# Optimization experiments

Measured on AMD Instinct MI355X. Metric: run time of the kernel, lower is better.

The kernel has to match this reference:

```python
import jax, jax.numpy as jnp
import numpy as np

B, S, H = 2, 1024, 2880
I = 2880
E = 16
K = 4


def setup_inputs() -> dict:
    key = jax.random.key(0)
    ks = jax.random.split(key, 4)
    sc = 0.02  # init scale to keep activations in a sane range
    return {
        "x": jax.random.normal(ks[0], (B, S, H), jnp.float32),
        "gate_w": jax.random.normal(ks[1], (E, H), jnp.float32) * sc,
        "gate_b": jnp.zeros((E,), jnp.float32),
        "w_gate_up": jax.random.normal(ks[2], (E, 2 * I, H), jnp.float32) * sc,
        "b_gate_up": jnp.zeros((E, 2 * I), jnp.float32),
        "w_down": jax.random.normal(ks[3], (E, H, I), jnp.float32) * sc,
        "b_down": jnp.zeros((E, H), jnp.float32),
        "swiglu_alpha": jnp.full((E,), 1.702, jnp.float32),
        "swiglu_beta": jnp.full((E,), 1.0, jnp.float32),
        "swiglu_limit": jnp.full((E,), 7.0, jnp.float32),
    }


def reference(x, gate_w, gate_b, w_gate_up, b_gate_up, w_down, b_down,
              swiglu_alpha, swiglu_beta, swiglu_limit):
    orig_shape = x.shape
    hidden = orig_shape[-1]
    t = x.reshape(-1, hidden)  # [T, H]
    T = t.shape[0]

    # Router: gate linear -> top-k -> renormalize via softmax over selected logits
    logits = t @ gate_w.T + gate_b  # [T, E]
    top_vals, top_idx = jax.lax.top_k(logits, K)  # [T, K]
    top_w = jax.nn.softmax(top_vals, axis=-1)  # RenormalizeMoeRoutingMethod
    # Dense combine matrix [T, E]; zero for non-selected experts
    combine = jnp.zeros((T, E), t.dtype).at[jnp.arange(T)[:, None], top_idx].set(top_w)

    def expert_body(acc, params):
        wgu, bgu, wd, bd, alpha, beta, lim, cw = params
        h = t @ wgu.T + bgu  # [T, 2I] fused gate_up
        glu, lin = jnp.split(h, 2, axis=-1)  # FUSED_GATE_UP_PROJ chunk
        glu = jnp.minimum(glu, lim)  # swiglu_limit clamp (gpt-oss)
        lin = jnp.clip(lin, -lim, lim)
        act = glu * jax.nn.sigmoid(alpha * glu) * (lin + beta)  # [T, I]
        y = act @ wd.T + bd  # [T, H]
        return acc + cw[:, None] * y, None

    init = jnp.zeros((T, hidden), t.dtype)
    out, _ = jax.lax.scan(
        expert_body, init,
        (w_gate_up, b_gate_up, w_down, b_down,
         swiglu_alpha, swiglu_beta, swiglu_limit, combine.T))
    return out.reshape(orig_shape)
```

## Files before the change

### kernel.cpp

```cpp
#include <hip/hip_runtime.h>
#include <stdint.h>
#include <math.h>

#define T_TOK 2048
#define H_DIM 2880
#define I_DIM 2880
#define E_NUM 16
#define TOPK 4

#define BT 256
#define BK 64
#define NK 45
#define MT_MAX 8
#define NT1 45
#define NT2 45

typedef __bf16 bf16_t;
typedef __bf16 bf16x8 __attribute__((ext_vector_type(8)));
typedef __bf16 bf16x4 __attribute__((ext_vector_type(4)));
typedef float f32x4 __attribute__((ext_vector_type(4)));

#define WAITV(N) asm volatile("s_waitcnt vmcnt(" #N ")" ::: "memory")
#define WAITL()  asm volatile("s_waitcnt lgkmcnt(0)" ::: "memory")
#define BAR()    asm volatile("s_barrier" ::: "memory")

__device__ __forceinline__ void gload16(const bf16_t* g, bf16_t* l) {
  __builtin_amdgcn_global_load_lds(
      (__attribute__((address_space(1))) const uint32_t*)g,
      (__attribute__((address_space(3))) uint32_t*)l, 16, 0, 0);
}

__device__ __forceinline__ f32x4 mfma16(bf16x8 a, bf16x8 b, f32x4 c) {
  return __builtin_amdgcn_mfma_f32_16x16x32_bf16(a, b, c, 0, 0, 0);
}

__global__ void k_prep(const float* __restrict__ x, bf16_t* __restrict__ xbf,
                       int* __restrict__ counts) {
  if (blockIdx.x == 0 && threadIdx.x < E_NUM) counts[threadIdx.x] = 0;
  int idx = blockIdx.x * 256 + threadIdx.x;
  const int total = T_TOK * H_DIM / 8;
  if (idx < total) {
    f32x4 a = ((const f32x4*)x)[2 * idx];
    f32x4 b = ((const f32x4*)x)[2 * idx + 1];
    bf16x8 o = {(bf16_t)a[0], (bf16_t)a[1], (bf16_t)a[2], (bf16_t)a[3],
                (bf16_t)b[0], (bf16_t)b[1], (bf16_t)b[2], (bf16_t)b[3]};
    ((bf16x8*)xbf)[idx] = o;
  }
}

__global__ void k_router(const float* __restrict__ x, const float* __restrict__ gw,
                         const float* __restrict__ gb, float* __restrict__ topw,
                         int* __restrict__ counts, int* __restrict__ rowsl) {
  const int t = blockIdx.x;
  const int lane = threadIdx.x;
  const int c = lane >> 4, e = lane & 15;
  const f32x4* x4 = (const f32x4*)(x + (size_t)t * H_DIM);
  const f32x4* w4 = (const f32x4*)(gw + (size_t)e * H_DIM);
  float p = 0.f;
  const int per = (H_DIM / 4) / 4;
  for (int i = c * per; i < (c + 1) * per; ++i) {
    f32x4 xv = x4[i], wv = w4[i];
    p += xv[0] * wv[0] + xv[1] * wv[1] + xv[2] * wv[2] + xv[3] * wv[3];
  }
  p += __shfl_xor(p, 16);
  p += __shfl_xor(p, 32);
  p += gb[e];
  __shared__ float lg[E_NUM];
  if (lane < E_NUM) lg[lane] = p;
  __syncthreads();
  if (lane == 0) {
    float v[E_NUM];
    #pragma unroll
    for (int i = 0; i < E_NUM; ++i) v[i] = lg[i];
    int idxs[TOPK]; float vals[TOPK];
    for (int k = 0; k < TOPK; ++k) {
      int bi = 0; float bv = -1e30f;
      for (int i = 0; i < E_NUM; ++i) {
        if (v[i] > bv) { bv = v[i]; bi = i; }
      }
      idxs[k] = bi; vals[k] = bv; v[bi] = -1e30f;
    }
    float m = vals[0], s = 0.f, w[TOPK];
    for (int k = 0; k < TOPK; ++k) { w[k] = expf(vals[k] - m); s += w[k]; }
    for (int k = 0; k < TOPK; ++k) {
      int slot = t * TOPK + k;
      topw[slot] = w[k] / s;
      int pos = atomicAdd(&counts[idxs[k]], 1);
      rowsl[idxs[k] * T_TOK + pos] = slot;
    }
  }
}


#define G_STAGE_T(KT, BUF) do {                                         \
    int c1_ = (KT) > (NK - 1) ? (NK - 1) : (KT);                        \
    _Pragma("unroll")                                                   \
    for (int i_ = 0; i_ < 4; ++i_)                                      \
      gload16(tsrc[i_] + c1_ * BK, &sT[BUF][wv * 2048 + i_ * 512]);     \
  } while (0)

#define G1_MFMA(CUR) do {                                               \
    _Pragma("unroll")                                                   \
    for (int ks = 0; ks < 2; ++ks) {                                    \
      const int koff = ks * 32 + (lane >> 4) * 8;                       \
      bf16x8 wg_[2], wl_[2], tf[4];                                     \
      _Pragma("unroll")                                                 \
      for (int wi = 0; wi < 2; ++wi) {                                  \
        int rg = 32 * wm + 16 * wi + (lane & 15);                       \
        int swz = koff ^ ((rg & 7) << 3);                               \
        wg_[wi] = *(const bf16x8*)(&sW[CUR][rg * 64 + swz]);            \
        wl_[wi] = *(const bf16x8*)(&sW[CUR][(rg + 64) * 64 + swz]);     \
      }                                                                 \
      _Pragma("unroll")                                                 \
      for (int tj = 0; tj < 4; ++tj) {                                  \
        int rt = 64 * wt + 16 * tj + (lane & 15);                       \
        tf[tj] = *(const bf16x8*)(&sT[CUR][rt * 64 + (koff ^ ((rt & 7) << 3))]); \
      }                                                                 \
      _Pragma("unroll")                                                 \
      for (int wi = 0; wi < 2; ++wi)                                    \
        _Pragma("unroll")                                               \
        for (int tj = 0; tj < 4; ++tj) {                                \
          accg[wi][tj] = mfma16(wg_[wi], tf[tj], accg[wi][tj]);         \
          accl[wi][tj] = mfma16(wl_[wi], tf[tj], accl[wi][tj]);         \
        }                                                               \
    }                                                                   \
  } while (0)

#define G1_ITER(KK, WSET) do {                                          \
    const int cur_ = (KK) & 1;                                          \
    G_STAGE_T((KK) + 1, cur_ ^ 1);                                      \
    _Pragma("unroll")                                                   \
    for (int p_ = 0; p_ < 4; ++p_) {                                    \
      bf16x4 b_ = {(bf16_t)WSET[p_][0], (bf16_t)WSET[p_][1],            \
                   (bf16_t)WSET[p_][2], (bf16_t)WSET[p_][3]};           \
      *(bf16x4*)(&sW[cur_ ^ 1][wo[p_]]) = b_;                           \
    }                                                                   \
    { int c3_ = (KK) + 3 > (NK - 1) ? (NK - 1) : (KK) + 3;              \
      _Pragma("unroll")                                                 \
      for (int p_ = 0; p_ < 4; ++p_)                                    \
        WSET[p_] = *(const f32x4*)(wbase + wgo[p_] + c3_ * BK); }       \
    __builtin_amdgcn_s_setprio(1);                                      \
    G1_MFMA(cur_);                                                      \
    __builtin_amdgcn_s_setprio(0);                                      \
    WAITV(4); WAITL(); BAR();                                           \
  } while (0)

__global__ __launch_bounds__(512, 2)
void k_gemm1(const bf16_t* __restrict__ xbf, const float* __restrict__ wgu,
             const float* __restrict__ bgu, const float* __restrict__ al,
             const float* __restrict__ be, const float* __restrict__ lim_,
             const int* __restrict__ counts, const int* __restrict__ rowsl,
             bf16_t* __restrict__ act) {
  const int nwg = E_NUM * NT1 * MT_MAX;
  const int L = (blockIdx.x & 7) * (nwg >> 3) + (blockIdx.x >> 3);
  const int mt = L & (MT_MAX - 1);
  const int t2 = L >> 3;
  const int nt = t2 % NT1;
  const int e  = t2 / NT1;
  const int Ne = counts[e];
  const int m0 = mt * BT;
  if (m0 >= Ne) return;
  const int n0 = nt * 64;

  __shared__ alignas(16) bf16_t sW[2][128 * 64];
  __shared__ alignas(16) bf16_t sT[2][256 * 64];

  const int tid = threadIdx.x;
  const int wv = tid >> 6, lane = tid & 63;
  const int wm = wv & 1, wt = wv >> 1;
  const int* rl = rowsl + e * T_TOK;

  const bf16_t* tsrc[4];
  {
    const int r_ = lane >> 3, cc = lane & 7;
    #pragma unroll
    for (int i = 0; i < 4; ++i) {
      int r = wv * 32 + i * 8 + r_;
      int li = m0 + r; if (li > Ne - 1) li = Ne - 1;
      int tok = rl[li] >> 2;
      tsrc[i] = xbf + (size_t)tok * H_DIM + ((cc ^ (r_ & 7)) << 3);
    }
  }

  const int wrow = tid >> 4, wf = tid & 15;
  const float* wbase = wgu + (size_t)e * (2 * I_DIM) * H_DIM + wf * 4;
  int wgo[4], wo[4];
  #pragma unroll
  for (int p = 0; p < 4; ++p) {
    int row = wrow + p * 32;
    int grow = (row < 64) ? (n0 + row) : (I_DIM + n0 + row - 64);
    wgo[p] = grow * H_DIM;
    wo[p] = row * 64 + ((wf * 4) ^ ((row & 7) << 3));
  }

  f32x4 zero = {0.f, 0.f, 0.f, 0.f};
  f32x4 accg[2][4], accl[2][4];
  #pragma unroll
  for (int i = 0; i < 2; ++i)
    #pragma unroll
    for (int j = 0; j < 4; ++j) { accg[i][j] = zero; accl[i][j] = zero; }

  f32x4 wA[4], wB[4];
  #pragma unroll
  for (int p = 0; p < 4; ++p) wA[p] = *(const f32x4*)(wbase + wgo[p]);
  WAITV(0);
  #pragma unroll
  for (int p = 0; p < 4; ++p) {
    bf16x4 b = {(bf16_t)wA[p][0], (bf16_t)wA[p][1],
                (bf16_t)wA[p][2], (bf16_t)wA[p][3]};
    *(bf16x4*)(&sW[0][wo[p]]) = b;
  }
  G_STAGE_T(0, 0);
  #pragma unroll
  for (int p = 0; p < 4; ++p) wA[p] = *(const f32x4*)(wbase + wgo[p] + 1 * BK);
  #pragma unroll
  for (int p = 0; p < 4; ++p) wB[p] = *(const f32x4*)(wbase + wgo[p] + 2 * BK);
  WAITV(4);
  WAITL(); BAR();

  for (int kb = 0; kb < NK - 1; kb += 2) {
    G1_ITER(kb, wA);
    G1_ITER(kb + 1, wB);
  }
  G1_ITER(NK - 1, wA);

  const float alpha = al[e], beta = be[e], lim = lim_[e];
  const float* bgp = bgu + (size_t)e * (2 * I_DIM);
  #pragma unroll
  for (int wi = 0; wi < 2; ++wi) {
    const int nb = n0 + 32 * wm + 16 * wi + ((lane >> 4) << 2);
    f32x4 bg4 = *(const f32x4*)(bgp + nb);
    f32x4 bl4 = *(const f32x4*)(bgp + I_DIM + nb);
    #pragma unroll
    for (int tj = 0; tj < 4; ++tj) {
      const int li2 = m0 + 64 * wt + 16 * tj + (lane & 15);
      if (li2 < Ne) {
        const int slot = rl[li2];
        bf16x4 ov;
        #pragma unroll
        for (int r = 0; r < 4; ++r) {
          float g = accg[wi][tj][r] + bg4[r];
          float l = accl[wi][tj][r] + bl4[r];
          g = fminf(g, lim);
          l = fminf(fmaxf(l, -lim), lim);
          float sg = 1.0f / (1.0f + expf(-alpha * g));
          ov[r] = (bf16_t)(g * sg * (l + beta));
        }
        *(bf16x4*)(&act[(size_t)slot * I_DIM + nb]) = ov;
      }
    }
  }
}


#define G2_MFMA(CUR) do {                                               \
    _Pragma("unroll")                                                   \
    for (int ks = 0; ks < 2; ++ks) {                                    \
      const int koff = ks * 32 + (lane >> 4) * 8;                       \
      bf16x8 wf_[2], tf[4];                                             \
      _Pragma("unroll")                                                 \
      for (int wi = 0; wi < 2; ++wi) {                                  \
        int rg = 32 * wm + 16 * wi + (lane & 15);                       \
        wf_[wi] = *(const bf16x8*)(&sW[CUR][rg * 64 + (koff ^ ((rg & 7) << 3))]); \
      }                                                                 \
      _Pragma("unroll")                                                 \
      for (int tj = 0; tj < 4; ++tj) {                                  \
        int rt = 64 * wt + 16 * tj + (lane & 15);                       \
        tf[tj] = *(const bf16x8*)(&sT[CUR][rt * 64 + (koff ^ ((rt & 7) << 3))]); \
      }                                                                 \
      _Pragma("unroll")                                                 \
      for (int wi = 0; wi < 2; ++wi)                                    \
        _Pragma("unroll")                                               \
        for (int tj = 0; tj < 4; ++tj)                                  \
          acc[wi][tj] = mfma16(wf_[wi], tf[tj], acc[wi][tj]);           \
    }                                                                   \
  } while (0)

#define G2_ITER(KK, WSET) do {                                          \
    const int cur_ = (KK) & 1;                                          \
    G_STAGE_T((KK) + 1, cur_ ^ 1);                                      \
    _Pragma("unroll")                                                   \
    for (int p_ = 0; p_ < 2; ++p_) {                                    \
      bf16x4 b_ = {(bf16_t)WSET[p_][0], (bf16_t)WSET[p_][1],            \
                   (bf16_t)WSET[p_][2], (bf16_t)WSET[p_][3]};           \
      *(bf16x4*)(&sW[cur_ ^ 1][wo[p_]]) = b_;                           \
    }                                                                   \
    { int c3_ = (KK) + 3 > (NK - 1) ? (NK - 1) : (KK) + 3;              \
      _Pragma("unroll")                                                 \
      for (int p_ = 0; p_ < 2; ++p_)                                    \
        WSET[p_] = *(const f32x4*)(wbase + wgo[p_] + c3_ * BK); }       \
    __builtin_amdgcn_s_setprio(1);                                      \
    G2_MFMA(cur_);                                                      \
    __builtin_amdgcn_s_setprio(0);                                      \
    WAITV(2); WAITL(); BAR();                                           \
  } while (0)

__global__ __launch_bounds__(512, 4)
void k_gemm2(const bf16_t* __restrict__ act, const float* __restrict__ wd,
             const float* __restrict__ bd, const float* __restrict__ topw,
             const int* __restrict__ counts, const int* __restrict__ rowsl,
             float* __restrict__ ybuf) {
  const int nwg = E_NUM * NT2 * MT_MAX;
  const int L = (blockIdx.x & 7) * (nwg >> 3) + (blockIdx.x >> 3);
  const int mt = L & (MT_MAX - 1);
  const int t2 = L >> 3;
  const int ht = t2 % NT2;
  const int e  = t2 / NT2;
  const int Ne = counts[e];
  const int m0 = mt * BT;
  if (m0 >= Ne) return;
  const int h0 = ht * 64;

  __shared__ alignas(16) bf16_t sW[2][64 * 64];
  __shared__ alignas(16) bf16_t sT[2][256 * 64];

  const int tid = threadIdx.x;
  const int wv = tid >> 6, lane = tid & 63;
  const int wm = wv & 1, wt = wv >> 1;
  const int* rl = rowsl + e * T_TOK;

  const bf16_t* tsrc[4];
  {
    const int r_ = lane >> 3, cc = lane & 7;
    #pragma unroll
    for (int i = 0; i < 4; ++i) {
      int r = wv * 32 + i * 8 + r_;
      int li = m0 + r; if (li > Ne - 1) li = Ne - 1;
      int slot = rl[li];
      tsrc[i] = act + (size_t)slot * I_DIM + ((cc ^ (r_ & 7)) << 3);
    }
  }

  const int wrow = tid >> 4, wf = tid & 15;
  const float* wbase = wd + (size_t)e * H_DIM * I_DIM + wf * 4;
  int wgo[2], wo[2];
  #pragma unroll
  for (int p = 0; p < 2; ++p) {
    int row = wrow + p * 32;
    wgo[p] = (h0 + row) * I_DIM;
    wo[p] = row * 64 + ((wf * 4) ^ ((row & 7) << 3));
  }

  f32x4 zero = {0.f, 0.f, 0.f, 0.f};
  f32x4 acc[2][4];
  #pragma unroll
  for (int i = 0; i < 2; ++i)
    #pragma unroll
    for (int j = 0; j < 4; ++j) acc[i][j] = zero;

  f32x4 wA[2], wB[2];
  #pragma unroll
  for (int p = 0; p < 2; ++p) wA[p] = *(const f32x4*)(wbase + wgo[p]);
  WAITV(0);
  #pragma unroll
  for (int p = 0; p < 2; ++p) {
    bf16x4 b = {(bf16_t)wA[p][0], (bf16_t)wA[p][1],
                (bf16_t)wA[p][2], (bf16_t)wA[p][3]};
    *(bf16x4*)(&sW[0][wo[p]]) = b;
  }
  G_STAGE_T(0, 0);
  #pragma unroll
  for (int p = 0; p < 2; ++p) wA[p] = *(const f32x4*)(wbase + wgo[p] + 1 * BK);
  #pragma unroll
  for (int p = 0; p < 2; ++p) wB[p] = *(const f32x4*)(wbase + wgo[p] + 2 * BK);
  WAITV(2);
  WAITL(); BAR();

  for (int kb = 0; kb < NK - 1; kb += 2) {
    G2_ITER(kb, wA);
    G2_ITER(kb + 1, wB);
  }
  G2_ITER(NK - 1, wA);

  const float* bdp = bd + (size_t)e * H_DIM;
  #pragma unroll
  for (int wi = 0; wi < 2; ++wi) {
    const int hb = h0 + 32 * wm + 16 * wi + ((lane >> 4) << 2);
    f32x4 b4 = *(const f32x4*)(bdp + hb);
    #pragma unroll
    for (int tj = 0; tj < 4; ++tj) {
      const int li2 = m0 + 64 * wt + 16 * tj + (lane & 15);
      if (li2 < Ne) {
        const int slot = rl[li2];
        const float tw = topw[slot];
        f32x4 o = (acc[wi][tj] + b4) * tw;
        *(f32x4*)(&ybuf[(size_t)slot * H_DIM + hb]) = o;
      }
    }
  }
}

__global__ void k_combine(const float* __restrict__ ybuf, float* __restrict__ out) {
  const int j4 = H_DIM / 4;
  int idx = blockIdx.x * 256 + threadIdx.x;
  if (idx >= T_TOK * j4) return;
  int t = idx / j4, j = idx - t * j4;
  const f32x4* yb = (const f32x4*)ybuf;
  f32x4 s = yb[(size_t)(t * 4 + 0) * j4 + j];
  s = s + yb[(size_t)(t * 4 + 1) * j4 + j];
  s = s + yb[(size_t)(t * 4 + 2) * j4 + j];
  s = s + yb[(size_t)(t * 4 + 3) * j4 + j];
  ((f32x4*)out)[idx] = s;
}

extern "C" void kernel_launch(void* const* d_in, const int* in_sizes, int n_in,
                              void* d_out, int out_size, void* d_ws, size_t ws_size,
                              hipStream_t stream) {
  const float* x   = (const float*)d_in[0];
  const float* gw  = (const float*)d_in[1];
  const float* gb  = (const float*)d_in[2];
  const float* wgu = (const float*)d_in[3];
  const float* bgu = (const float*)d_in[4];
  const float* wd  = (const float*)d_in[5];
  const float* bd  = (const float*)d_in[6];
  const float* sal = (const float*)d_in[7];
  const float* sbe = (const float*)d_in[8];
  const float* sli = (const float*)d_in[9];
  float* out = (float*)d_out;

  char* ws = (char*)d_ws;
  int*    counts = (int*)(ws + 0);
  int*    rowsl  = (int*)(ws + 4096);
  float*  topw   = (float*)(ws + 4096 + 131072);
  bf16_t* xbf    = (bf16_t*)(ws + (1 << 20));
  bf16_t* act    = (bf16_t*)(ws + (size_t)(16 << 20));
  float*  ybuf   = (float*)(ws + (size_t)(64 << 20));

  k_prep<<<dim3(2880), dim3(256), 0, stream>>>(x, xbf, counts);
  k_router<<<dim3(T_TOK), dim3(64), 0, stream>>>(x, gw, gb, topw, counts, rowsl);
  k_gemm1<<<dim3(E_NUM * NT1 * MT_MAX), dim3(512), 0, stream>>>(
      xbf, wgu, bgu, sal, sbe, sli, counts, rowsl, act);
  k_gemm2<<<dim3(E_NUM * NT2 * MT_MAX), dim3(512), 0, stream>>>(
      act, wd, bd, topw, counts, rowsl, ybuf);
  k_combine<<<dim3(5760), dim3(256), 0, stream>>>(ybuf, out);
}
```

Measured before the change: 1.546 ms.

## Shrink GEMM tiles to 128 tokens, K=32, triple-buffer token tiles, new LDS swizzle

Both grouped expert GEMMs move from 256-token, 512-thread tiles with K-step 64 to 128-token, 256-thread tiles with K-step 32. Token tiles are now triple-buffered with a prefetch distance of two steps, under a new LDS swizzle function. The main loop is unrolled by six to rotate the buffers. The aim is less wasted work on partially filled expert tiles, more resident workgroups per CU, and deeper latency hiding. In exchange there are twice as many barriers per K, and the fp32 weights are re-read by more token tiles.

New measurement: 3.890 ms. +151.6%, slower.

```diff
diff --git a/kernel.cpp b/kernel.cpp
--- a/kernel.cpp
+++ b/kernel.cpp
@@ -8,10 +8,10 @@
 #define E_NUM 16
 #define TOPK 4
 
-#define BT 256
-#define BK 64
-#define NK 45
-#define MT_MAX 8
+#define BT 128
+#define BK 32
+#define NK 90
+#define MT_MAX 16
 #define NT1 45
 #define NT2 45
 
@@ -32,6 +32,11 @@
 
 __device__ __forceinline__ f32x4 mfma16(bf16x8 a, bf16x8 b, f32x4 c) {
   return __builtin_amdgcn_mfma_f32_16x16x32_bf16(a, b, c, 0, 0, 0);
+}
+
+__device__ __forceinline__ int ldsoff(int row, int g) {
+  int r = row & 31;
+  return ((row >> 5) << 10) + (((r << 2) + ((g + (r >> 1)) & 3)) << 3);
 }
 
 __global__ void k_prep(const float* __restrict__ x, bf16_t* __restrict__ xbf,
@@ -91,61 +96,56 @@
   }
 }
 
-
 #define G_STAGE_T(KT, BUF) do {                                         \
     int c1_ = (KT) > (NK - 1) ? (NK - 1) : (KT);                        \
     _Pragma("unroll")                                                   \
-    for (int i_ = 0; i_ < 4; ++i_)                                      \
-      gload16(tsrc[i_] + c1_ * BK, &sT[BUF][wv * 2048 + i_ * 512]);     \
+    for (int i_ = 0; i_ < 2; ++i_)                                      \
+      gload16(tsrc[i_] + c1_ * BK, &sT[BUF][wv * 1024 + i_ * 512]);     \
   } while (0)
 
-#define G1_MFMA(CUR) do {                                               \
-    _Pragma("unroll")                                                   \
-    for (int ks = 0; ks < 2; ++ks) {                                    \
-      const int koff = ks * 32 + (lane >> 4) * 8;                       \
-      bf16x8 wg_[2], wl_[2], tf[4];                                     \
-      _Pragma("unroll")                                                 \
-      for (int wi = 0; wi < 2; ++wi) {                                  \
-        int rg = 32 * wm + 16 * wi + (lane & 15);                       \
-        int swz = koff ^ ((rg & 7) << 3);                               \
-        wg_[wi] = *(const bf16x8*)(&sW[CUR][rg * 64 + swz]);            \
-        wl_[wi] = *(const bf16x8*)(&sW[CUR][(rg + 64) * 64 + swz]);     \
-      }                                                                 \
+
+#define G1_MFMA(SWC, STR) do {                                          \
+    const int g_ = lane >> 4, rs_ = lane & 15;                          \
+    bf16x8 wg_[2], wl_[2], tf[4];                                       \
+    _Pragma("unroll")                                                   \
+    for (int wi = 0; wi < 2; ++wi) {                                    \
+      int rg = 32 * wm + 16 * wi + rs_;                                 \
+      wg_[wi] = *(const bf16x8*)(&sW[SWC][ldsoff(rg, g_)]);             \
+      wl_[wi] = *(const bf16x8*)(&sW[SWC][ldsoff(rg + 64, g_)]);        \
+    }                                                                   \
+    _Pragma("unroll")                                                   \
+    for (int tj = 0; tj < 4; ++tj) {                                    \
+      int rt = 64 * wt + 16 * tj + rs_;                                 \
+      tf[tj] = *(const bf16x8*)(&sT[STR][ldsoff(rt, g_)]);              \
+    }                                                                   \
+    _Pragma("unroll")                                                   \
+    for (int wi = 0; wi < 2; ++wi)                                      \
       _Pragma("unroll")                                                 \
       for (int tj = 0; tj < 4; ++tj) {                                  \
-        int rt = 64 * wt + 16 * tj + (lane & 15);                       \
-        tf[tj] = *(const bf16x8*)(&sT[CUR][rt * 64 + (koff ^ ((rt & 7) << 3))]); \
+        accg[wi][tj] = mfma16(wg_[wi], tf[tj], accg[wi][tj]);           \
+        accl[wi][tj] = mfma16(wl_[wi], tf[tj], accl[wi][tj]);           \
       }                                                                 \
-      _Pragma("unroll")                                                 \
-      for (int wi = 0; wi < 2; ++wi)                                    \
-        _Pragma("unroll")                                               \
-        for (int tj = 0; tj < 4; ++tj) {                                \
-          accg[wi][tj] = mfma16(wg_[wi], tf[tj], accg[wi][tj]);         \
-          accl[wi][tj] = mfma16(wl_[wi], tf[tj], accl[wi][tj]);         \
-        }                                                               \
-    }                                                                   \
   } while (0)
 
-#define G1_ITER(KK, WSET) do {                                          \
-    const int cur_ = (KK) & 1;                                          \
-    G_STAGE_T((KK) + 1, cur_ ^ 1);                                      \
+#define G1_ITER(KK, WSET, SWC, STR, STW) do {                           \
+    G_STAGE_T((KK) + 2, STW);                                           \
     _Pragma("unroll")                                                   \
     for (int p_ = 0; p_ < 4; ++p_) {                                    \
       bf16x4 b_ = {(bf16_t)WSET[p_][0], (bf16_t)WSET[p_][1],            \
                    (bf16_t)WSET[p_][2], (bf16_t)WSET[p_][3]};           \
-      *(bf16x4*)(&sW[cur_ ^ 1][wo[p_]]) = b_;                           \
+      *(bf16x4*)(&sW[(SWC) ^ 1][wo[p_]]) = b_;                          \
     }                                                                   \
     { int c3_ = (KK) + 3 > (NK - 1) ? (NK - 1) : (KK) + 3;              \
       _Pragma("unroll")                                                 \
       for (int p_ = 0; p_ < 4; ++p_)                                    \
         WSET[p_] = *(const f32x4*)(wbase + wgo[p_] + c3_ * BK); }       \
     __builtin_amdgcn_s_setprio(1);                                      \
-    G1_MFMA(cur_);                                                      \
+    G1_MFMA(SWC, STR);                                                  \
     __builtin_amdgcn_s_setprio(0);                                      \
-    WAITV(4); WAITL(); BAR();                                           \
+    WAITV(6); WAITL(); BAR();                                           \
   } while (0)
 
-__global__ __launch_bounds__(512, 2)
+__global__ __launch_bounds__(256, 4)
 void k_gemm1(const bf16_t* __restrict__ xbf, const float* __restrict__ wgu,
              const float* __restrict__ bgu, const float* __restrict__ al,
              const float* __restrict__ be, const float* __restrict__ lim_,
@@ -154,7 +154,7 @@
   const int nwg = E_NUM * NT1 * MT_MAX;
   const int L = (blockIdx.x & 7) * (nwg >> 3) + (blockIdx.x >> 3);
   const int mt = L & (MT_MAX - 1);
-  const int t2 = L >> 3;
+  const int t2 = L >> 4;
   const int nt = t2 % NT1;
   const int e  = t2 / NT1;
   const int Ne = counts[e];
@@ -162,35 +162,36 @@
   if (m0 >= Ne) return;
   const int n0 = nt * 64;
 
-  __shared__ alignas(16) bf16_t sW[2][128 * 64];
-  __shared__ alignas(16) bf16_t sT[2][256 * 64];
+  __shared__ alignas(16) bf16_t sW[2][128 * 32];
+  __shared__ alignas(16) bf16_t sT[3][128 * 32];
 
   const int tid = threadIdx.x;
   const int wv = tid >> 6, lane = tid & 63;
   const int wm = wv & 1, wt = wv >> 1;
   const int* rl = rowsl + e * T_TOK;
 
-  const bf16_t* tsrc[4];
+  const bf16_t* tsrc[2];
   {
-    const int r_ = lane >> 3, cc = lane & 7;
-    #pragma unroll
-    for (int i = 0; i < 4; ++i) {
-      int r = wv * 32 + i * 8 + r_;
-      int li = m0 + r; if (li > Ne - 1) li = Ne - 1;
+    #pragma unroll
+    for (int i = 0; i < 2; ++i) {
+      int q = i * 64 + lane;
+      int r = q >> 2;
+      int g = ((q & 3) - (r >> 1)) & 3;
+      int li = m0 + wv * 32 + r; if (li > Ne - 1) li = Ne - 1;
       int tok = rl[li] >> 2;
-      tsrc[i] = xbf + (size_t)tok * H_DIM + ((cc ^ (r_ & 7)) << 3);
-    }
-  }
-
-  const int wrow = tid >> 4, wf = tid & 15;
-  const float* wbase = wgu + (size_t)e * (2 * I_DIM) * H_DIM + wf * 4;
+      tsrc[i] = xbf + (size_t)tok * H_DIM + g * 8;
+    }
+  }
+
+  const int wrow = tid >> 3, wf2 = tid & 7;
+  const float* wbase = wgu + (size_t)e * (2 * I_DIM) * H_DIM + wf2 * 4;
   int wgo[4], wo[4];
   #pragma unroll
   for (int p = 0; p < 4; ++p) {
     int row = wrow + p * 32;
     int grow = (row < 64) ? (n0 + row) : (I_DIM + n0 + row - 64);
     wgo[p] = grow * H_DIM;
-    wo[p] = row * 64 + ((wf * 4) ^ ((row & 7) << 3));
+    wo[p] = ldsoff(row, wf2 >> 1) + (wf2 & 1) * 4;
   }
 
   f32x4 zero = {0.f, 0.f, 0.f, 0.f};
@@ -212,17 +213,21 @@
   }
   G_STAGE_T(0, 0);
   #pragma unroll
-  for (int p = 0; p < 4; ++p) wA[p] = *(const f32x4*)(wbase + wgo[p] + 1 * BK);
+  for (int p = 0; p < 4; ++p) wA[p] = *(const f32x4*)(wbase + wgo[p] + BK);
+  WAITV(0);
+  G_STAGE_T(1, 1);
   #pragma unroll
   for (int p = 0; p < 4; ++p) wB[p] = *(const f32x4*)(wbase + wgo[p] + 2 * BK);
-  WAITV(4);
   WAITL(); BAR();
 
-  for (int kb = 0; kb < NK - 1; kb += 2) {
-    G1_ITER(kb, wA);
-    G1_ITER(kb + 1, wB);
-  }
-  G1_ITER(NK - 1, wA);
+  for (int kb = 0; kb < NK; kb += 6) {
+    G1_ITER(kb + 0, wA, 0, 0, 2);
+    G1_ITER(kb + 1, wB, 1, 1, 0);
+    G1_ITER(kb + 2, wA, 0, 2, 1);
+    G1_ITER(kb + 3, wB, 1, 0, 2);
+    G1_ITER(kb + 4, wA, 0, 1, 0);
+    G1_ITER(kb + 5, wB, 1, 2, 1);
+  }
 
   const float alpha = al[e], beta = be[e], lim = lim_[e];
   const float* bgp = bgu + (size_t)e * (2 * I_DIM);
@@ -253,49 +258,45 @@
 }
 
 
-#define G2_MFMA(CUR) do {                                               \
-    _Pragma("unroll")                                                   \
-    for (int ks = 0; ks < 2; ++ks) {                                    \
-      const int koff = ks * 32 + (lane >> 4) * 8;                       \
-      bf16x8 wf_[2], tf[4];                                             \
+#define G2_MFMA(SWC, STR) do {                                          \
+    const int g_ = lane >> 4, rs_ = lane & 15;                          \
+    bf16x8 wf_[2], tf[4];                                               \
+    _Pragma("unroll")                                                   \
+    for (int wi = 0; wi < 2; ++wi) {                                    \
+      int rg = 32 * wm + 16 * wi + rs_;                                 \
+      wf_[wi] = *(const bf16x8*)(&sW[SWC][ldsoff(rg, g_)]);             \
+    }                                                                   \
+    _Pragma("unroll")                                                   \
+    for (int tj = 0; tj < 4; ++tj) {                                    \
+      int rt = 64 * wt + 16 * tj + rs_;                                 \
+      tf[tj] = *(const bf16x8*)(&sT[STR][ldsoff(rt, g_)]);              \
+    }                                                                   \
+    _Pragma("unroll")                                                   \
+    for (int wi = 0; wi < 2; ++wi)                                      \
       _Pragma("unroll")                                                 \
-      for (int wi = 0; wi < 2; ++wi) {                                  \
-        int rg = 32 * wm + 16 * wi + (lane & 15);                       \
-        wf_[wi] = *(const bf16x8*)(&sW[CUR][rg * 64 + (koff ^ ((rg & 7) << 3))]); \
-      }                                                                 \
-      _Pragma("unroll")                                                 \
-      for (int tj = 0; tj < 4; ++tj) {                                  \
-        int rt = 64 * wt + 16 * tj + (lane & 15);                       \
-        tf[tj] = *(const bf16x8*)(&sT[CUR][rt * 64 + (koff ^ ((rt & 7) << 3))]); \
-      }                                                                 \
-      _Pragma("unroll")                                                 \
-      for (int wi = 0; wi < 2; ++wi)                                    \
-        _Pragma("unroll")                                               \
-        for (int tj = 0; tj < 4; ++tj)                                  \
-          acc[wi][tj] = mfma16(wf_[wi], tf[tj], acc[wi][tj]);           \
-    }                                                                   \
+      for (int tj = 0; tj < 4; ++tj)                                    \
+        acc[wi][tj] = mfma16(wf_[wi], tf[tj], acc[wi][tj]);             \
   } while (0)
 
-#define G2_ITER(KK, WSET) do {                                          \
-    const int cur_ = (KK) & 1;                                          \
-    G_STAGE_T((KK) + 1, cur_ ^ 1);                                      \
+#define G2_ITER(KK, WSET, SWC, STR, STW) do {                           \
+    G_STAGE_T((KK) + 2, STW);                                           \
     _Pragma("unroll")                                                   \
     for (int p_ = 0; p_ < 2; ++p_) {                                    \
       bf16x4 b_ = {(bf16_t)WSET[p_][0], (bf16_t)WSET[p_][1],            \
                    (bf16_t)WSET[p_][2], (bf16_t)WSET[p_][3]};           \
-      *(bf16x4*)(&sW[cur_ ^ 1][wo[p_]]) = b_;                           \
+      *(bf16x4*)(&sW[(SWC) ^ 1][wo[p_]]) = b_;                          \
     }                                                                   \
     { int c3_ = (KK) + 3 > (NK - 1) ? (NK - 1) : (KK) + 3;              \
       _Pragma("unroll")                                                 \
       for (int p_ = 0; p_ < 2; ++p_)                                    \
         WSET[p_] = *(const f32x4*)(wbase + wgo[p_] + c3_ * BK); }       \
     __builtin_amdgcn_s_setprio(1);                                      \
-    G2_MFMA(cur_);                                                      \
+    G2_MFMA(SWC, STR);                                                  \
     __builtin_amdgcn_s_setprio(0);                                      \
-    WAITV(2); WAITL(); BAR();                                           \
+    WAITV(4); WAITL(); BAR();                                           \
   } while (0)
 
-__global__ __launch_bounds__(512, 4)
+__global__ __launch_bounds__(256, 4)
 void k_gemm2(const bf16_t* __restrict__ act, const float* __restrict__ wd,
              const float* __restrict__ bd, const float* __restrict__ topw,
              const int* __restrict__ counts, const int* __restrict__ rowsl,
@@ -303,7 +304,7 @@
   const int nwg = E_NUM * NT2 * MT_MAX;
   const int L = (blockIdx.x & 7) * (nwg >> 3) + (blockIdx.x >> 3);
   const int mt = L & (MT_MAX - 1);
-  const int t2 = L >> 3;
+  const int t2 = L >> 4;
   const int ht = t2 % NT2;
   const int e  = t2 / NT2;
   const int Ne = counts[e];
@@ -311,34 +312,35 @@
   if (m0 >= Ne) return;
   const int h0 = ht * 64;
 
-  __shared__ alignas(16) bf16_t sW[2][64 * 64];
-  __shared__ alignas(16) bf16_t sT[2][256 * 64];
+  __shared__ alignas(16) bf16_t sW[2][64 * 32];
+  __shared__ alignas(16) bf16_t sT[3][128 * 32];
 
   const int tid = threadIdx.x;
   const int wv = tid >> 6, lane = tid & 63;
   const int wm = wv & 1, wt = wv >> 1;
   const int* rl = rowsl + e * T_TOK;
 
-  const bf16_t* tsrc[4];
+  const bf16_t* tsrc[2];
   {
-    const int r_ = lane >> 3, cc = lane & 7;
-    #pragma unroll
-    for (int i = 0; i < 4; ++i) {
-      int r = wv * 32 + i * 8 + r_;
-      int li = m0 + r; if (li > Ne - 1) li = Ne - 1;
+    #pragma unroll
+    for (int i = 0; i < 2; ++i) {
+      int q = i * 64 + lane;
+      int r = q >> 2;
+      int g = ((q & 3) - (r >> 1)) & 3;
+      int li = m0 + wv * 32 + r; if (li > Ne - 1) li = Ne - 1;
       int slot = rl[li];
-      tsrc[i] = act + (size_t)slot * I_DIM + ((cc ^ (r_ & 7)) << 3);
-    }
-  }
-
-  const int wrow = tid >> 4, wf = tid & 15;
-  const float* wbase = wd + (size_t)e * H_DIM * I_DIM + wf * 4;
+      tsrc[i] = act + (size_t)slot * I_DIM + g * 8;
+    }
+  }
+
+  const int wrow = tid >> 3, wf2 = tid & 7;
+  const float* wbase = wd + (size_t)e * H_DIM * I_DIM + wf2 * 4;
   int wgo[2], wo[2];
   #pragma unroll
   for (int p = 0; p < 2; ++p) {
     int row = wrow + p * 32;
     wgo[p] = (h0 + row) * I_DIM;
-    wo[p] = row * 64 + ((wf * 4) ^ ((row & 7) << 3));
+    wo[p] = ldsoff(row, wf2 >> 1) + (wf2 & 1) * 4;
   }
 
   f32x4 zero = {0.f, 0.f, 0.f, 0.f};
@@ -360,17 +362,21 @@
   }
   G_STAGE_T(0, 0);
   #pragma unroll
-  for (int p = 0; p < 2; ++p) wA[p] = *(const f32x4*)(wbase + wgo[p] + 1 * BK);
+  for (int p = 0; p < 2; ++p) wA[p] = *(const f32x4*)(wbase + wgo[p] + BK);
+  WAITV(0);
+  G_STAGE_T(1, 1);
   #pragma unroll
   for (int p = 0; p < 2; ++p) wB[p] = *(const f32x4*)(wbase + wgo[p] + 2 * BK);
-  WAITV(2);
   WAITL(); BAR();
 
-  for (int kb = 0; kb < NK - 1; kb += 2) {
-    G2_ITER(kb, wA);
-    G2_ITER(kb + 1, wB);
-  }
-  G2_ITER(NK - 1, wA);
+  for (int kb = 0; kb < NK; kb += 6) {
+    G2_ITER(kb + 0, wA, 0, 0, 2);
+    G2_ITER(kb + 1, wB, 1, 1, 0);
+    G2_ITER(kb + 2, wA, 0, 2, 1);
+    G2_ITER(kb + 3, wB, 1, 0, 2);
+    G2_ITER(kb + 4, wA, 0, 1, 0);
+    G2_ITER(kb + 5, wB, 1, 2, 1);
+  }
 
   const float* bdp = bd + (size_t)e * H_DIM;
   #pragma unroll
@@ -428,9 +434,9 @@
 
   k_prep<<<dim3(2880), dim3(256), 0, stream>>>(x, xbf, counts);
   k_router<<<dim3(T_TOK), dim3(64), 0, stream>>>(x, gw, gb, topw, counts, rowsl);
-  k_gemm1<<<dim3(E_NUM * NT1 * MT_MAX), dim3(512), 0, stream>>>(
+  k_gemm1<<<dim3(E_NUM * NT1 * MT_MAX), dim3(256), 0, stream>>>(
       xbf, wgu, bgu, sal, sbe, sli, counts, rowsl, act);
-  k_gemm2<<<dim3(E_NUM * NT2 * MT_MAX), dim3(512), 0, stream>>>(
+  k_gemm2<<<dim3(E_NUM * NT2 * MT_MAX), dim3(256), 0, stream>>>(
       act, wd, bd, topw, counts, rowsl, ybuf);
   k_combine<<<dim3(5760), dim3(256), 0, stream>>>(ybuf, out);
 }
```

## Enlarge GEMM N-tiles and use 1024-thread blocks with new LDS swizzle

Applied to the files above, without the earlier changes.

Both expert GEMMs now run with 16 waves per block. The gate_up kernel's weight tile grows from 64 to 96 columns per half (192 rows), and the down kernel's from 64 to 192 output columns. With larger N-tiles, each block re-reads the gathered token rows fewer times, and the fp32 weights are loaded and converted fewer times per token. The LDS layout switches from an XOR swizzle to a rotation-based one (loff) with per-lane global_load_lds addressing. The cost is more LDS per block, higher register pressure from the larger accumulators, and launch bounds of 1024x4 that may not be satisfiable and could force spills or lower occupancy.

Result: faster. 1.465 ms (-5.2%).

```diff
diff --git a/kernel.cpp b/kernel.cpp
--- a/kernel.cpp
+++ b/kernel.cpp
@@ -12,8 +12,8 @@
 #define BK 64
 #define NK 45
 #define MT_MAX 8
-#define NT1 45
-#define NT2 45
+#define NT1 30
+#define NT2 15
 
 typedef __bf16 bf16_t;
 typedef __bf16 bf16x8 __attribute__((ext_vector_type(8)));
@@ -24,7 +24,7 @@
 #define WAITL()  asm volatile("s_waitcnt lgkmcnt(0)" ::: "memory")
 #define BAR()    asm volatile("s_barrier" ::: "memory")
 
-__device__ __forceinline__ void gload16(const bf16_t* g, bf16_t* l) {
+__device__ __forceinline__ void gload16(const void* g, void* l) {
   __builtin_amdgcn_global_load_lds(
       (__attribute__((address_space(1))) const uint32_t*)g,
       (__attribute__((address_space(3))) uint32_t*)l, 16, 0, 0);
@@ -32,6 +32,15 @@
 
 __device__ __forceinline__ f32x4 mfma16(bf16x8 a, bf16x8 b, f32x4 c) {
   return __builtin_amdgcn_mfma_f32_16x16x32_bf16(a, b, c, 0, 0, 0);
+}
+
+__device__ __forceinline__ int loff(int row, int g) {
+  return ((row >> 5) << 11) + ((row & 31) << 6) + (((g + (row & 7)) & 7) << 3);
+}
+
+__device__ __forceinline__ bf16x4 cvt4(f32x4 a) {
+  bf16x4 o = {(bf16_t)a[0], (bf16_t)a[1], (bf16_t)a[2], (bf16_t)a[3]};
+  return o;
 }
 
 __global__ void k_prep(const float* __restrict__ x, bf16_t* __restrict__ xbf,
@@ -91,37 +100,37 @@
   }
 }
 
-
 #define G_STAGE_T(KT, BUF) do {                                         \
     int c1_ = (KT) > (NK - 1) ? (NK - 1) : (KT);                        \
     _Pragma("unroll")                                                   \
-    for (int i_ = 0; i_ < 4; ++i_)                                      \
-      gload16(tsrc[i_] + c1_ * BK, &sT[BUF][wv * 2048 + i_ * 512]);     \
+    for (int i_ = 0; i_ < 2; ++i_)                                      \
+      gload16(tsrc[i_] + c1_ * BK,                                      \
+              &sT[BUF][wv * 1024 + i_ * 512 + lane * 8]);               \
   } while (0)
+
 
 #define G1_MFMA(CUR) do {                                               \
     _Pragma("unroll")                                                   \
     for (int ks = 0; ks < 2; ++ks) {                                    \
-      const int koff = ks * 32 + (lane >> 4) * 8;                       \
-      bf16x8 wg_[2], wl_[2], tf[4];                                     \
-      _Pragma("unroll")                                                 \
-      for (int wi = 0; wi < 2; ++wi) {                                  \
-        int rg = 32 * wm + 16 * wi + (lane & 15);                       \
-        int swz = koff ^ ((rg & 7) << 3);                               \
-        wg_[wi] = *(const bf16x8*)(&sW[CUR][rg * 64 + swz]);            \
-        wl_[wi] = *(const bf16x8*)(&sW[CUR][(rg + 64) * 64 + swz]);     \
+      const int gk = 4 * ks + u;                                        \
+      bf16x8 wg_[3], wl_[3], tf[2];                                     \
+      _Pragma("unroll")                                                 \
+      for (int f = 0; f < 3; ++f) {                                     \
+        int rg = 48 * wo + 16 * f + rs;                                 \
+        wg_[f] = *(const bf16x8*)(&sW[CUR][loff(rg, gk)]);              \
+        wl_[f] = *(const bf16x8*)(&sW[CUR][loff(rg + 96, gk)]);         \
       }                                                                 \
       _Pragma("unroll")                                                 \
-      for (int tj = 0; tj < 4; ++tj) {                                  \
-        int rt = 64 * wt + 16 * tj + (lane & 15);                       \
-        tf[tj] = *(const bf16x8*)(&sT[CUR][rt * 64 + (koff ^ ((rt & 7) << 3))]); \
+      for (int tj = 0; tj < 2; ++tj) {                                  \
+        int rt = 32 * wt + 16 * tj + rs;                                \
+        tf[tj] = *(const bf16x8*)(&sT[CUR][loff(rt, gk)]);              \
       }                                                                 \
       _Pragma("unroll")                                                 \
-      for (int wi = 0; wi < 2; ++wi)                                    \
+      for (int f = 0; f < 3; ++f)                                       \
         _Pragma("unroll")                                               \
-        for (int tj = 0; tj < 4; ++tj) {                                \
-          accg[wi][tj] = mfma16(wg_[wi], tf[tj], accg[wi][tj]);         \
-          accl[wi][tj] = mfma16(wl_[wi], tf[tj], accl[wi][tj]);         \
+        for (int tj = 0; tj < 2; ++tj) {                                \
+          accg[f][tj] = mfma16(wg_[f], tf[tj], accg[f][tj]);            \
+          accl[f][tj] = mfma16(wl_[f], tf[tj], accl[f][tj]);            \
         }                                                               \
     }                                                                   \
   } while (0)
@@ -130,22 +139,19 @@
     const int cur_ = (KK) & 1;                                          \
     G_STAGE_T((KK) + 1, cur_ ^ 1);                                      \
     _Pragma("unroll")                                                   \
-    for (int p_ = 0; p_ < 4; ++p_) {                                    \
-      bf16x4 b_ = {(bf16_t)WSET[p_][0], (bf16_t)WSET[p_][1],            \
-                   (bf16_t)WSET[p_][2], (bf16_t)WSET[p_][3]};           \
-      *(bf16x4*)(&sW[cur_ ^ 1][wo[p_]]) = b_;                           \
-    }                                                                   \
+    for (int p_ = 0; p_ < 3; ++p_)                                      \
+      *(bf16x4*)(&sW[cur_ ^ 1][woff[p_]]) = cvt4(WSET[p_]);             \
     { int c3_ = (KK) + 3 > (NK - 1) ? (NK - 1) : (KK) + 3;              \
       _Pragma("unroll")                                                 \
-      for (int p_ = 0; p_ < 4; ++p_)                                    \
-        WSET[p_] = *(const f32x4*)(wbase + wgo[p_] + c3_ * BK); }       \
+      for (int p_ = 0; p_ < 3; ++p_)                                    \
+        WSET[p_] = *(const f32x4*)(wsrc[p_] + c3_ * BK); }              \
     __builtin_amdgcn_s_setprio(1);                                      \
     G1_MFMA(cur_);                                                      \
     __builtin_amdgcn_s_setprio(0);                                      \
-    WAITV(4); WAITL(); BAR();                                           \
+    WAITV(3); WAITL(); BAR();                                           \
   } while (0)
 
-__global__ __launch_bounds__(512, 2)
+__global__ __launch_bounds__(1024, 4)
 void k_gemm1(const bf16_t* __restrict__ xbf, const float* __restrict__ wgu,
              const float* __restrict__ bgu, const float* __restrict__ al,
              const float* __restrict__ be, const float* __restrict__ lim_,
@@ -160,62 +166,61 @@
   const int Ne = counts[e];
   const int m0 = mt * BT;
   if (m0 >= Ne) return;
-  const int n0 = nt * 64;
-
-  __shared__ alignas(16) bf16_t sW[2][128 * 64];
+  const int n0 = nt * 96;
+
+  __shared__ alignas(16) bf16_t sW[2][192 * 64];
   __shared__ alignas(16) bf16_t sT[2][256 * 64];
 
   const int tid = threadIdx.x;
   const int wv = tid >> 6, lane = tid & 63;
-  const int wm = wv & 1, wt = wv >> 1;
+  const int wt = wv & 7, wo = wv >> 3;
+  const int u = lane >> 4, rs = lane & 15;
   const int* rl = rowsl + e * T_TOK;
 
-  const bf16_t* tsrc[4];
+  const bf16_t* tsrc[2];
   {
-    const int r_ = lane >> 3, cc = lane & 7;
-    #pragma unroll
-    for (int i = 0; i < 4; ++i) {
-      int r = wv * 32 + i * 8 + r_;
-      int li = m0 + r; if (li > Ne - 1) li = Ne - 1;
+    #pragma unroll
+    for (int i = 0; i < 2; ++i) {
+      int q = i * 64 + lane;
+      int row = 16 * wv + (q >> 3);
+      int gd = q & 7;
+      int g = (gd - (row & 7)) & 7;
+      int li = m0 + row; if (li > Ne - 1) li = Ne - 1;
       int tok = rl[li] >> 2;
-      tsrc[i] = xbf + (size_t)tok * H_DIM + ((cc ^ (r_ & 7)) << 3);
+      tsrc[i] = xbf + (size_t)tok * H_DIM + g * 8;
     }
   }
 
   const int wrow = tid >> 4, wf = tid & 15;
-  const float* wbase = wgu + (size_t)e * (2 * I_DIM) * H_DIM + wf * 4;
-  int wgo[4], wo[4];
-  #pragma unroll
-  for (int p = 0; p < 4; ++p) {
-    int row = wrow + p * 32;
-    int grow = (row < 64) ? (n0 + row) : (I_DIM + n0 + row - 64);
-    wgo[p] = grow * H_DIM;
-    wo[p] = row * 64 + ((wf * 4) ^ ((row & 7) << 3));
+  const float* wsrc[3];
+  int woff[3];
+  #pragma unroll
+  for (int p = 0; p < 3; ++p) {
+    int row = 64 * p + wrow;
+    int grow = (row < 96) ? (n0 + row) : (I_DIM + n0 + row - 96);
+    wsrc[p] = wgu + ((size_t)e * 2 * I_DIM + grow) * H_DIM + wf * 4;
+    woff[p] = loff(row, wf >> 1) + (wf & 1) * 4;
   }
 
   f32x4 zero = {0.f, 0.f, 0.f, 0.f};
-  f32x4 accg[2][4], accl[2][4];
-  #pragma unroll
-  for (int i = 0; i < 2; ++i)
-    #pragma unroll
-    for (int j = 0; j < 4; ++j) { accg[i][j] = zero; accl[i][j] = zero; }
-
-  f32x4 wA[4], wB[4];
-  #pragma unroll
-  for (int p = 0; p < 4; ++p) wA[p] = *(const f32x4*)(wbase + wgo[p]);
+  f32x4 accg[3][2], accl[3][2];
+  #pragma unroll
+  for (int i = 0; i < 3; ++i)
+    #pragma unroll
+    for (int j = 0; j < 2; ++j) { accg[i][j] = zero; accl[i][j] = zero; }
+
+  f32x4 wA[3], wB[3];
+  #pragma unroll
+  for (int p = 0; p < 3; ++p) wA[p] = *(const f32x4*)(wsrc[p]);
   WAITV(0);
   #pragma unroll
-  for (int p = 0; p < 4; ++p) {
-    bf16x4 b = {(bf16_t)wA[p][0], (bf16_t)wA[p][1],
-                (bf16_t)wA[p][2], (bf16_t)wA[p][3]};
-    *(bf16x4*)(&sW[0][wo[p]]) = b;
-  }
+  for (int p = 0; p < 3; ++p) *(bf16x4*)(&sW[0][woff[p]]) = cvt4(wA[p]);
   G_STAGE_T(0, 0);
   #pragma unroll
-  for (int p = 0; p < 4; ++p) wA[p] = *(const f32x4*)(wbase + wgo[p] + 1 * BK);
-  #pragma unroll
-  for (int p = 0; p < 4; ++p) wB[p] = *(const f32x4*)(wbase + wgo[p] + 2 * BK);
-  WAITV(4);
+  for (int p = 0; p < 3; ++p) wA[p] = *(const f32x4*)(wsrc[p] + BK);
+  #pragma unroll
+  for (int p = 0; p < 3; ++p) wB[p] = *(const f32x4*)(wsrc[p] + 2 * BK);
+  WAITV(3);
   WAITL(); BAR();
 
   for (int kb = 0; kb < NK - 1; kb += 2) {
@@ -227,20 +232,20 @@
   const float alpha = al[e], beta = be[e], lim = lim_[e];
   const float* bgp = bgu + (size_t)e * (2 * I_DIM);
   #pragma unroll
-  for (int wi = 0; wi < 2; ++wi) {
-    const int nb = n0 + 32 * wm + 16 * wi + ((lane >> 4) << 2);
+  for (int f = 0; f < 3; ++f) {
+    const int nb = n0 + 48 * wo + 16 * f + 4 * u;
     f32x4 bg4 = *(const f32x4*)(bgp + nb);
     f32x4 bl4 = *(const f32x4*)(bgp + I_DIM + nb);
     #pragma unroll
-    for (int tj = 0; tj < 4; ++tj) {
-      const int li2 = m0 + 64 * wt + 16 * tj + (lane & 15);
+    for (int tj = 0; tj < 2; ++tj) {
+      const int li2 = m0 + 32 * wt + 16 * tj + rs;
       if (li2 < Ne) {
         const int slot = rl[li2];
         bf16x4 ov;
         #pragma unroll
         for (int r = 0; r < 4; ++r) {
-          float g = accg[wi][tj][r] + bg4[r];
-          float l = accl[wi][tj][r] + bl4[r];
+          float g = accg[f][tj][r] + bg4[r];
+          float l = accl[f][tj][r] + bl4[r];
           g = fminf(g, lim);
           l = fminf(fmaxf(l, -lim), lim);
           float sg = 1.0f / (1.0f + expf(-alpha * g));
@@ -256,23 +261,23 @@
 #define G2_MFMA(CUR) do {                                               \
     _Pragma("unroll")                                                   \
     for (int ks = 0; ks < 2; ++ks) {                                    \
-      const int koff = ks * 32 + (lane >> 4) * 8;                       \
-      bf16x8 wf_[2], tf[4];                                             \
-      _Pragma("unroll")                                                 \
-      for (int wi = 0; wi < 2; ++wi) {                                  \
-        int rg = 32 * wm + 16 * wi + (lane & 15);                       \
-        wf_[wi] = *(const bf16x8*)(&sW[CUR][rg * 64 + (koff ^ ((rg & 7) << 3))]); \
+      const int gk = 4 * ks + u;                                        \
+      bf16x8 wf_[6], tf[2];                                             \
+      _Pragma("unroll")                                                 \
+      for (int f = 0; f < 6; ++f) {                                     \
+        int rg = 96 * wo + 16 * f + rs;                                 \
+        wf_[f] = *(const bf16x8*)(&sW[CUR][loff(rg, gk)]);              \
       }                                                                 \
       _Pragma("unroll")                                                 \
-      for (int tj = 0; tj < 4; ++tj) {                                  \
-        int rt = 64 * wt + 16 * tj + (lane & 15);                       \
-        tf[tj] = *(const bf16x8*)(&sT[CUR][rt * 64 + (koff ^ ((rt & 7) << 3))]); \
+      for (int tj = 0; tj < 2; ++tj) {                                  \
+        int rt = 32 * wt + 16 * tj + rs;                                \
+        tf[tj] = *(const bf16x8*)(&sT[CUR][loff(rt, gk)]);              \
       }                                                                 \
       _Pragma("unroll")                                                 \
-      for (int wi = 0; wi < 2; ++wi)                                    \
+      for (int f = 0; f < 6; ++f)                                       \
         _Pragma("unroll")                                               \
-        for (int tj = 0; tj < 4; ++tj)                                  \
-          acc[wi][tj] = mfma16(wf_[wi], tf[tj], acc[wi][tj]);           \
+        for (int tj = 0; tj < 2; ++tj)                                  \
+          acc[f][tj] = mfma16(wf_[f], tf[tj], acc[f][tj]);              \
     }                                                                   \
   } while (0)
 
@@ -280,22 +285,19 @@
     const int cur_ = (KK) & 1;                                          \
     G_STAGE_T((KK) + 1, cur_ ^ 1);                                      \
     _Pragma("unroll")                                                   \
-    for (int p_ = 0; p_ < 2; ++p_) {                                    \
-      bf16x4 b_ = {(bf16_t)WSET[p_][0], (bf16_t)WSET[p_][1],            \
-                   (bf16_t)WSET[p_][2], (bf16_t)WSET[p_][3]};           \
-      *(bf16x4*)(&sW[cur_ ^ 1][wo[p_]]) = b_;                           \
-    }                                                                   \
+    for (int p_ = 0; p_ < 3; ++p_)                                      \
+      *(bf16x4*)(&sW[cur_ ^ 1][woff[p_]]) = cvt4(WSET[p_]);             \
     { int c3_ = (KK) + 3 > (NK - 1) ? (NK - 1) : (KK) + 3;              \
       _Pragma("unroll")                                                 \
-      for (int p_ = 0; p_ < 2; ++p_)                                    \
-        WSET[p_] = *(const f32x4*)(wbase + wgo[p_] + c3_ * BK); }       \
+      for (int p_ = 0; p_ < 3; ++p_)                                    \
+        WSET[p_] = *(const f32x4*)(wsrc[p_] + c3_ * BK); }              \
     __builtin_amdgcn_s_setprio(1);                                      \
     G2_MFMA(cur_);                                                      \
     __builtin_amdgcn_s_setprio(0);                                      \
-    WAITV(2); WAITL(); BAR();                                           \
+    WAITV(3); WAITL(); BAR();                                           \
   } while (0)
 
-__global__ __launch_bounds__(512, 4)
+__global__ __launch_bounds__(1024, 4)
 void k_gemm2(const bf16_t* __restrict__ act, const float* __restrict__ wd,
              const float* __restrict__ bd, const float* __restrict__ topw,
              const int* __restrict__ counts, const int* __restrict__ rowsl,
@@ -309,62 +311,60 @@
   const int Ne = counts[e];
   const int m0 = mt * BT;
   if (m0 >= Ne) return;
-  const int h0 = ht * 64;
-
-  __shared__ alignas(16) bf16_t sW[2][64 * 64];
+  const int h0 = ht * 192;
+
+  __shared__ alignas(16) bf16_t sW[2][192 * 64];
   __shared__ alignas(16) bf16_t sT[2][256 * 64];
 
   const int tid = threadIdx.x;
   const int wv = tid >> 6, lane = tid & 63;
-  const int wm = wv & 1, wt = wv >> 1;
+  const int wt = wv & 7, wo = wv >> 3;
+  const int u = lane >> 4, rs = lane & 15;
   const int* rl = rowsl + e * T_TOK;
 
-  const bf16_t* tsrc[4];
+  const bf16_t* tsrc[2];
   {
-    const int r_ = lane >> 3, cc = lane & 7;
-    #pragma unroll
-    for (int i = 0; i < 4; ++i) {
-      int r = wv * 32 + i * 8 + r_;
-      int li = m0 + r; if (li > Ne - 1) li = Ne - 1;
+    #pragma unroll
+    for (int i = 0; i < 2; ++i) {
+      int q = i * 64 + lane;
+      int row = 16 * wv + (q >> 3);
+      int gd = q & 7;
+      int g = (gd - (row & 7)) & 7;
+      int li = m0 + row; if (li > Ne - 1) li = Ne - 1;
       int slot = rl[li];
-      tsrc[i] = act + (size_t)slot * I_DIM + ((cc ^ (r_ & 7)) << 3);
+      tsrc[i] = act + (size_t)slot * I_DIM + g * 8;
     }
   }
 
   const int wrow = tid >> 4, wf = tid & 15;
-  const float* wbase = wd + (size_t)e * H_DIM * I_DIM + wf * 4;
-  int wgo[2], wo[2];
-  #pragma unroll
-  for (int p = 0; p < 2; ++p) {
-    int row = wrow + p * 32;
-    wgo[p] = (h0 + row) * I_DIM;
-    wo[p] = row * 64 + ((wf * 4) ^ ((row & 7) << 3));
+  const float* wsrc[3];
+  int woff[3];
+  #pragma unroll
+  for (int p = 0; p < 3; ++p) {
+    int row = 64 * p + wrow;
+    wsrc[p] = wd + ((size_t)e * H_DIM + (h0 + row)) * I_DIM + wf * 4;
+    woff[p] = loff(row, wf >> 1) + (wf & 1) * 4;
   }
 
   f32x4 zero = {0.f, 0.f, 0.f, 0.f};
-  f32x4 acc[2][4];
-  #pragma unroll
-  for (int i = 0; i < 2; ++i)
-    #pragma unroll
-    for (int j = 0; j < 4; ++j) acc[i][j] = zero;
-
-  f32x4 wA[2], wB[2];
-  #pragma unroll
-  for (int p = 0; p < 2; ++p) wA[p] = *(const f32x4*)(wbase + wgo[p]);
+  f32x4 acc[6][2];
+  #pragma unroll
+  for (int i = 0; i < 6; ++i)
+    #pragma unroll
+    for (int j = 0; j < 2; ++j) acc[i][j] = zero;
+
+  f32x4 wA[3], wB[3];
+  #pragma unroll
+  for (int p = 0; p < 3; ++p) wA[p] = *(const f32x4*)(wsrc[p]);
   WAITV(0);
   #pragma unroll
-  for (int p = 0; p < 2; ++p) {
-    bf16x4 b = {(bf16_t)wA[p][0], (bf16_t)wA[p][1],
-                (bf16_t)wA[p][2], (bf16_t)wA[p][3]};
-    *(bf16x4*)(&sW[0][wo[p]]) = b;
-  }
+  for (int p = 0; p < 3; ++p) *(bf16x4*)(&sW[0][woff[p]]) = cvt4(wA[p]);
   G_STAGE_T(0, 0);
   #pragma unroll
-  for (int p = 0; p < 2; ++p) wA[p] = *(const f32x4*)(wbase + wgo[p] + 1 * BK);
-  #pragma unroll
-  for (int p = 0; p < 2; ++p) wB[p] = *(const f32x4*)(wbase + wgo[p] + 2 * BK);
-  WAITV(2);
-  WAITL(); BAR();
+  for (int p = 0; p < 3; ++p) wA[p] = *(const f32x4*)(wsrc[p] + BK);
+  #pragma unroll
+  for (int p = 0; p < 3; ++p) wB[p] = *(const f32x4*)(wsrc[p] + 2 * BK);
+  WAITV(3); WAITL(); BAR();
 
   for (int kb = 0; kb < NK - 1; kb += 2) {
     G2_ITER(kb, wA);
@@ -374,16 +374,16 @@
 
   const float* bdp = bd + (size_t)e * H_DIM;
   #pragma unroll
-  for (int wi = 0; wi < 2; ++wi) {
-    const int hb = h0 + 32 * wm + 16 * wi + ((lane >> 4) << 2);
+  for (int f = 0; f < 6; ++f) {
+    const int hb = h0 + 96 * wo + 16 * f + 4 * u;
     f32x4 b4 = *(const f32x4*)(bdp + hb);
     #pragma unroll
-    for (int tj = 0; tj < 4; ++tj) {
-      const int li2 = m0 + 64 * wt + 16 * tj + (lane & 15);
+    for (int tj = 0; tj < 2; ++tj) {
+      const int li2 = m0 + 32 * wt + 16 * tj + rs;
       if (li2 < Ne) {
         const int slot = rl[li2];
         const float tw = topw[slot];
-        f32x4 o = (acc[wi][tj] + b4) * tw;
+        f32x4 o = (acc[f][tj] + b4) * tw;
         *(f32x4*)(&ybuf[(size_t)slot * H_DIM + hb]) = o;
       }
     }
@@ -428,9 +428,9 @@
 
   k_prep<<<dim3(2880), dim3(256), 0, stream>>>(x, xbf, counts);
   k_router<<<dim3(T_TOK), dim3(64), 0, stream>>>(x, gw, gb, topw, counts, rowsl);
-  k_gemm1<<<dim3(E_NUM * NT1 * MT_MAX), dim3(512), 0, stream>>>(
+  k_gemm1<<<dim3(E_NUM * NT1 * MT_MAX), dim3(1024), 0, stream>>>(
       xbf, wgu, bgu, sal, sbe, sli, counts, rowsl, act);
-  k_gemm2<<<dim3(E_NUM * NT2 * MT_MAX), dim3(512), 0, stream>>>(
+  k_gemm2<<<dim3(E_NUM * NT2 * MT_MAX), dim3(1024), 0, stream>>>(
       act, wd, bd, topw, counts, rowsl, ybuf);
   k_combine<<<dim3(5760), dim3(256), 0, stream>>>(ybuf, out);
 }
```
